# Optimization experiments

Hardware: AMD Instinct MI355X
Metric: run time of the kernel (lower is better)

Reference implementation:

```python
import jax, jax.numpy as jnp
import numpy as np

DEMBED = 512
DMODEL = 512
HEAD = 8
B, L = 4, 2048


def setup_inputs() -> dict:
    key = jax.random.key(0)
    ks = jax.random.split(key, 12)
    s_in = 1.0 / np.sqrt(DEMBED)
    s_out = 1.0 / np.sqrt(DMODEL)
    return {
        "x_q": jax.random.normal(ks[0], (B, L, DEMBED), jnp.float32),
        "x_k": jax.random.normal(ks[1], (B, L, DEMBED), jnp.float32),
        "x_v": jax.random.normal(ks[2], (B, L, DEMBED), jnp.float32),
        "mask": jax.random.randint(ks[3], (B, L, L), 0, 2, jnp.int32),
        "Wq": jax.random.uniform(ks[4], (DMODEL, DEMBED), jnp.float32, -s_in, s_in),
        "bq": jnp.zeros((DMODEL,), jnp.float32),
        "Wk": jax.random.uniform(ks[5], (DMODEL, DEMBED), jnp.float32, -s_in, s_in),
        "bk": jnp.zeros((DMODEL,), jnp.float32),
        "Wv": jax.random.uniform(ks[6], (DMODEL, DEMBED), jnp.float32, -s_in, s_in),
        "bv": jnp.zeros((DMODEL,), jnp.float32),
        "Wo": jax.random.uniform(ks[7], (DEMBED, DMODEL), jnp.float32, -s_out, s_out),
        "bo": jnp.zeros((DEMBED,), jnp.float32),
    }


def _split_heads(x):
    # [B, L, D] -> [B, head, L, h_dv]; head h gets contiguous channels h*h_dv:(h+1)*h_dv,
    # matching torch's transpose(1,2).reshape(B,head,h_dv,L).transpose(2,3)
    b, l, d = x.shape
    return x.reshape(b, l, HEAD, d // HEAD).transpose(0, 2, 1, 3)


def reference(x_q, x_k, x_v, mask, Wq, bq, Wk, bk, Wv, bv, Wo, bo):
    q = _split_heads(x_q @ Wq.T + bq)  # [B, H, L, hd]
    k = _split_heads(x_k @ Wk.T + bk)
    v = _split_heads(x_v @ Wv.T + bv)
    h_dv = q.shape[-1]
    scores = jnp.einsum("bhqd,bhkd->bhqk", q, k) / np.sqrt(h_dv)
    scores = scores + mask[:, None, :, :].astype(scores.dtype) * (-1e30)
    attn = jax.nn.softmax(scores, axis=-1)
    out = jnp.einsum("bhqk,bhkd->bhqd", attn, v)  # [B, H, L, hd]
    out = out.transpose(0, 2, 1, 3).reshape(x_q.shape[0], x_q.shape[1], DMODEL)
    final = out @ Wo.T + bo
    return final, attn
```

## Files before the change

### kernel.cpp

```cpp
#include <hip/hip_runtime.h>

typedef unsigned short u16;
typedef __attribute__((ext_vector_type(8))) short short8;
typedef __attribute__((ext_vector_type(4))) float f32x4;

#define DE 512
#define SL 2048
#define NB 4
#define NH 8
#define HD 64

__device__ __forceinline__ float bf2f(u16 h) {
    union { unsigned u; float f; } v; v.u = ((unsigned)h) << 16; return v.f;
}
__device__ __forceinline__ u16 f2bf(float f) {
    union { float f; unsigned u; } v; v.f = f;
    unsigned u = v.u;
    return (u16)((u + 0x7FFFu + ((u >> 16) & 1u)) >> 16);
}
__device__ __forceinline__ short8 ld8f(const float* __restrict__ p) {
    const float4 a = *(const float4*)p;
    const float4 b = *(const float4*)(p + 4);
    short8 r;
    ((u16*)&r)[0] = f2bf(a.x); ((u16*)&r)[1] = f2bf(a.y);
    ((u16*)&r)[2] = f2bf(a.z); ((u16*)&r)[3] = f2bf(a.w);
    ((u16*)&r)[4] = f2bf(b.x); ((u16*)&r)[5] = f2bf(b.y);
    ((u16*)&r)[6] = f2bf(b.z); ((u16*)&r)[7] = f2bf(b.w);
    return r;
}

__global__ __launch_bounds__(256) void cvt3(const float* __restrict__ s0,
                                            const float* __restrict__ s1,
                                            const float* __restrict__ s2,
                                            u16* __restrict__ dst, int per) {
    const float* src = (blockIdx.y == 0) ? s0 : ((blockIdx.y == 1) ? s1 : s2);
    const int idx = (blockIdx.x * 256 + threadIdx.x) * 8;
    if (idx >= per) return;
    short8 v = ld8f(src + idx);
    *(short8*)(dst + (size_t)blockIdx.y * per + idx) = v;
}

__device__ __forceinline__ void llds16(const u16* g, u16* l) {
    __builtin_amdgcn_global_load_lds((const __attribute__((address_space(1))) void*)g,
                                     (__attribute__((address_space(3))) void*)l, 16, 0, 0);
}

template <int MODE>
__global__ __launch_bounds__(256, 1) void gemm_lds(const u16* __restrict__ X,
                                                   const u16* __restrict__ W,
                                                   const float* __restrict__ bias,
                                                   void* __restrict__ outv) {
    __shared__ __align__(16) u16 As[2][8192];
    __shared__ __align__(16) u16 Bs[2][8192];

    const int tid = threadIdx.x;
    const int l = tid & 63, w = tid >> 6;
    const int q16 = l & 15, quad = l >> 4;
    const int tok0 = blockIdx.x * 128;
    const int col0 = blockIdx.y * 128;
    const int wr = w >> 1, wc = w & 1;

    const int srow = w * 8 + (l >> 3);
    const int scol = ((l & 7) ^ (l >> 3)) * 8;
    const u16* ga = X + (size_t)(tok0 + srow) * DE + scol;
    const u16* gb = W + (size_t)(col0 + srow) * DE + scol;
    u16* la0 = &As[0][tid * 8]; u16* la1 = &As[1][tid * 8];
    u16* lb0 = &Bs[0][tid * 8]; u16* lb1 = &Bs[1][tid * 8];

    f32x4 acc[4][4] = {};

    #pragma unroll
    for (int i = 0; i < 4; ++i) {
        llds16(ga + (size_t)i * 32 * DE, la0 + i * 2048);
        llds16(gb + (size_t)i * 32 * DE, lb0 + i * 2048);
    }
    __syncthreads();

    int cur = 0;
    for (int ks = 64; ks <= DE; ks += 64) {
        if (ks < DE) {
            u16* da = cur ? la0 : la1;
            u16* db = cur ? lb0 : lb1;
            #pragma unroll
            for (int i = 0; i < 4; ++i) {
                llds16(ga + (size_t)i * 32 * DE + ks, da + i * 2048);
                llds16(gb + (size_t)i * 32 * DE + ks, db + i * 2048);
            }
        }
        const char* Ab = (const char*)As[cur];
        const char* Bb = (const char*)Bs[cur];
        #pragma unroll
        for (int kk = 0; kk < 64; kk += 32) {
            short8 af[4], bf[4];
            #pragma unroll
            for (int m = 0; m < 4; ++m) {
                const int row = wr * 64 + m * 16 + q16;
                const int byt = row * 128 + (((kk + quad * 8) * 2) ^ ((q16 & 7) << 4));
                af[m] = *(const short8*)(Ab + byt);
            }
            #pragma unroll
            for (int n = 0; n < 4; ++n) {
                const int row = wc * 64 + n * 16 + q16;
                const int byt = row * 128 + (((kk + quad * 8) * 2) ^ ((q16 & 7) << 4));
                bf[n] = *(const short8*)(Bb + byt);
            }
            #pragma unroll
            for (int m = 0; m < 4; ++m)
                #pragma unroll
                for (int n = 0; n < 4; ++n)
                    acc[m][n] = __builtin_amdgcn_mfma_f32_16x16x32_bf16(af[m], bf[n], acc[m][n], 0, 0, 0);
        }
        __syncthreads();
        cur ^= 1;
    }

    #pragma unroll
    for (int n = 0; n < 4; ++n) {
        const int col = col0 + wc * 64 + n * 16 + q16;
        const float bv = bias[col];
        #pragma unroll
        for (int m = 0; m < 4; ++m) {
            const f32x4 a4 = acc[m][n];
            const int tg0 = tok0 + wr * 64 + m * 16 + quad * 4;
            if (MODE == 2) {
                const int b = tg0 >> 11, t0 = tg0 & 2047;
                const int h = col >> 6, d = col & 63;
                ushort4 pk;
                pk.x = f2bf(a4[0] + bv); pk.y = f2bf(a4[1] + bv);
                pk.z = f2bf(a4[2] + bv); pk.w = f2bf(a4[3] + bv);
                *(ushort4*)((u16*)outv + ((size_t)((b * NH + h) * HD + d) << 11) + t0) = pk;
            } else if (MODE == 1) {
                const int h = col >> 6, d = col & 63;
                #pragma unroll
                for (int r = 0; r < 4; ++r) {
                    const int tg = tg0 + r;
                    const int b = tg >> 11, t = tg & 2047;
                    ((u16*)outv)[(((size_t)(b * NH + h) * SL + t) << 6) + d] = f2bf(a4[r] + bv);
                }
            } else {
                #pragma unroll
                for (int r = 0; r < 4; ++r)
                    ((float*)outv)[(size_t)(tg0 + r) * DE + col] = a4[r] + bv;
            }
        }
    }
}

template <bool XBF, bool WBF, int MODE>
__global__ __launch_bounds__(256) void gemm512(const void* __restrict__ Xv,
                                               const void* __restrict__ Wv,
                                               const float* __restrict__ bias,
                                               void* __restrict__ outv) {
    const int lane = threadIdx.x & 63;
    const int wave = threadIdx.x >> 6;
    const int q16 = lane & 15, quad = lane >> 4;
    const int row0 = blockIdx.x * 64 + wave * 16;
    const int col0 = blockIdx.y * 64;

    f32x4 acc[4] = {};
    #pragma unroll 4
    for (int kk = 0; kk < DE; kk += 32) {
        short8 a;
        if (XBF)
            a = *(const short8*)((const u16*)Xv + (size_t)(row0 + q16) * DE + kk + quad * 8);
        else
            a = ld8f((const float*)Xv + (size_t)(row0 + q16) * DE + kk + quad * 8);
        #pragma unroll
        for (int ct = 0; ct < 4; ++ct) {
            short8 bw;
            if (WBF)
                bw = *(const short8*)((const u16*)Wv + (size_t)(col0 + ct * 16 + q16) * DE + kk + quad * 8);
            else
                bw = ld8f((const float*)Wv + (size_t)(col0 + ct * 16 + q16) * DE + kk + quad * 8);
            acc[ct] = __builtin_amdgcn_mfma_f32_16x16x32_bf16(a, bw, acc[ct], 0, 0, 0);
        }
    }
    #pragma unroll
    for (int ct = 0; ct < 4; ++ct) {
        const int col = col0 + ct * 16 + q16;
        const float bv = bias[col];
        #pragma unroll
        for (int r = 0; r < 4; ++r) {
            const int tg = row0 + quad * 4 + r;
            ((float*)outv)[(size_t)tg * DE + col] = acc[ct][r] + bv;
        }
    }
}

__global__ __launch_bounds__(512) void attn_kernel(const u16* __restrict__ Q,
                                                   const u16* __restrict__ K,
                                                   const u16* __restrict__ Vt,
                                                   const int* __restrict__ mask,
                                                   float* __restrict__ attn_out,
                                                   u16* __restrict__ Obuf) {
    __shared__ __align__(16) u16 P[16][2056];
    __shared__ float partial[16][8];
    __shared__ float linv[16];
    __shared__ float ored[4][16][16];

    const int tid = threadIdx.x;
    const int lane = tid & 63, wave = tid >> 6;
    const int q16 = lane & 15, quad = lane >> 4;
    const int qblk = blockIdx.x, h = blockIdx.y, b = blockIdx.z;
    const int qbase = qblk * 16;

    const u16* qplane = Q + (size_t)((b * NH + h) * SL) * HD;
    const u16* kplane = K + (size_t)((b * NH + h) * SL) * HD;

    const u16* qrow = qplane + (qbase + q16) * HD + quad * 8;
    const short8 aq0 = *(const short8*)(qrow);
    const short8 aq1 = *(const short8*)(qrow + 32);

    const int qg0 = qbase + quad * 4;
    const int* mbase = mask + (size_t)(b * SL + qg0) * SL;
    const int k0 = wave * 256;
    float rs0 = 0.f, rs1 = 0.f, rs2 = 0.f, rs3 = 0.f;
    #pragma unroll 2
    for (int kt = 0; kt < 16; ++kt) {
        const int kbase = k0 + kt * 16;
        const u16* krow = kplane + (kbase + q16) * HD + quad * 8;
        short8 b0 = *(const short8*)(krow);
        short8 b1 = *(const short8*)(krow + 32);
        f32x4 s = {};
        s = __builtin_amdgcn_mfma_f32_16x16x32_bf16(aq0, b0, s, 0, 0, 0);
        s = __builtin_amdgcn_mfma_f32_16x16x32_bf16(aq1, b1, s, 0, 0, 0);
        const int* mrow = mbase + kbase + q16;
        const float u0 = mrow[0]          ? 0.0f : __expf(s[0] * 0.125f);
        const float u1 = mrow[SL]         ? 0.0f : __expf(s[1] * 0.125f);
        const float u2 = mrow[2 * SL]     ? 0.0f : __expf(s[2] * 0.125f);
        const float u3 = mrow[3 * SL]     ? 0.0f : __expf(s[3] * 0.125f);
        rs0 += u0; rs1 += u1; rs2 += u2; rs3 += u3;
        P[quad * 4 + 0][kbase + q16] = f2bf(u0);
        P[quad * 4 + 1][kbase + q16] = f2bf(u1);
        P[quad * 4 + 2][kbase + q16] = f2bf(u2);
        P[quad * 4 + 3][kbase + q16] = f2bf(u3);
    }
    #pragma unroll
    for (int off = 1; off < 16; off <<= 1) {
        rs0 += __shfl_xor(rs0, off);
        rs1 += __shfl_xor(rs1, off);
        rs2 += __shfl_xor(rs2, off);
        rs3 += __shfl_xor(rs3, off);
    }
    if (q16 == 0) {
        partial[quad * 4 + 0][wave] = rs0;
        partial[quad * 4 + 1][wave] = rs1;
        partial[quad * 4 + 2][wave] = rs2;
        partial[quad * 4 + 3][wave] = rs3;
    }
    __syncthreads();

    if (tid < 16) {
        float s = 0.f;
        #pragma unroll
        for (int w = 0; w < 8; ++w) s += partial[tid][w];
        linv[tid] = 1.0f / s;
    }
    __syncthreads();

    {
        const int r3 = tid >> 5, cseg = tid & 31;
        const float inv = linv[r3];
        const size_t rowbase = ((size_t)((b * NH + h) * SL + qbase + r3)) * SL;
        #pragma unroll
        for (int i = 0; i < 8; ++i) {
            const int c = cseg * 8 + i * 256;
            short8 v = *(const short8*)&P[r3][c];
            f32x4 w0, w1;
            w0[0] = bf2f(((u16*)&v)[0]) * inv;
            w0[1] = bf2f(((u16*)&v)[1]) * inv;
            w0[2] = bf2f(((u16*)&v)[2]) * inv;
            w0[3] = bf2f(((u16*)&v)[3]) * inv;
            w1[0] = bf2f(((u16*)&v)[4]) * inv;
            w1[1] = bf2f(((u16*)&v)[5]) * inv;
            w1[2] = bf2f(((u16*)&v)[6]) * inv;
            w1[3] = bf2f(((u16*)&v)[7]) * inv;
            __builtin_nontemporal_store(w0, (f32x4*)(attn_out + rowbase + c));
            __builtin_nontemporal_store(w1, (f32x4*)(attn_out + rowbase + c + 4));
        }
    }

    const int dt = wave & 3, kh = wave >> 2;
    const u16* vplane = Vt + (size_t)((b * NH + h) * HD) * SL;
    f32x4 o = {};
    const int kstart = kh * 1024;
    #pragma unroll 4
    for (int kk = kstart; kk < kstart + 1024; kk += 32) {
        short8 a = *(const short8*)&P[q16][kk + quad * 8];
        short8 bv = *(const short8*)(vplane + (dt * 16 + q16) * SL + kk + quad * 8);
        o = __builtin_amdgcn_mfma_f32_16x16x32_bf16(a, bv, o, 0, 0, 0);
    }
    if (kh == 1) {
        #pragma unroll
        for (int rr = 0; rr < 4; ++rr) ored[dt][quad * 4 + rr][q16] = o[rr];
    }
    __syncthreads();
    if (kh == 0) {
        #pragma unroll
        for (int rr = 0; rr < 4; ++rr) {
            const int row = quad * 4 + rr;
            const float val = (o[rr] + ored[dt][row][q16]) * linv[row];
            const int qg = qbase + row;
            Obuf[(size_t)(b * SL + qg) * DE + h * HD + dt * 16 + q16] = f2bf(val);
        }
    }
}

extern "C" void kernel_launch(void* const* d_in, const int* in_sizes, int n_in,
                              void* d_out, int out_size, void* d_ws, size_t ws_size,
                              hipStream_t stream) {
    const float* x_q = (const float*)d_in[0];
    const float* x_k = (const float*)d_in[1];
    const float* x_v = (const float*)d_in[2];
    const int* mask = (const int*)d_in[3];
    const float* Wq = (const float*)d_in[4];
    const float* bq = (const float*)d_in[5];
    const float* Wk = (const float*)d_in[6];
    const float* bk = (const float*)d_in[7];
    const float* Wv = (const float*)d_in[8];
    const float* bv = (const float*)d_in[9];
    const float* Wo = (const float*)d_in[10];
    const float* bo = (const float*)d_in[11];

    u16* ws = (u16*)d_ws;
    u16* qb = ws;
    u16* kb = ws + 4194304;
    u16* vt = ws + 2 * 4194304;
    u16* ob = ws + 3 * 4194304;

    float* outp = (float*)d_out;
    float* attn_out = outp + 4194304;

    u16* xbf = (u16*)attn_out;
    u16* wbf = xbf + 3 * 4194304;

    cvt3<<<dim3(2048, 3), 256, 0, stream>>>(x_q, x_k, x_v, xbf, 4194304);
    cvt3<<<dim3(128, 3), 256, 0, stream>>>(Wq, Wk, Wv, wbf, 262144);

    dim3 gl(64, 4);
    gemm_lds<1><<<gl, 256, 0, stream>>>(xbf, wbf, bq, qb);
    gemm_lds<1><<<gl, 256, 0, stream>>>(xbf + 4194304, wbf + 262144, bk, kb);
    gemm_lds<2><<<gl, 256, 0, stream>>>(xbf + 2 * 4194304, wbf + 2 * 262144, bv, vt);

    attn_kernel<<<dim3(128, 8, 4), 512, 0, stream>>>(qb, kb, vt, mask, attn_out, ob);

    if (ws_size >= (size_t)34078720) {
        u16* wobf = ws + 4 * 4194304;
        cvt3<<<dim3(128, 1), 256, 0, stream>>>(Wo, Wo, Wo, wobf, 262144);
        gemm_lds<0><<<gl, 256, 0, stream>>>(ob, wobf, bo, outp);
    } else {
        gemm512<true, false, 0><<<dim3(128, 8), 256, 0, stream>>>(ob, Wo, bo, outp);
    }
}
```

Baseline: 891.0 us.

## Merge QKV projections into one launch with smaller 64x64 tiles

The three Q/K/V projection GEMMs become a single launch that uses blockIdx.z to pick the input, weight and bias. Output tiles shrink from 128x128 to 64x64, so each GEMM gets 1024 blocks instead of 256, and the launch-bounds minimum of one block per CU is dropped. The output projection now always uses the LDS-tiled bf16 path, with Wo converted into the freed Q buffer, replacing the older register-only fallback. The aim is to fill the GPU better and cut launch count, at the cost of lower per-block data reuse and more global traffic per FLOP.

```diff
diff --git a/kernel.cpp b/kernel.cpp
--- a/kernel.cpp
+++ b/kernel.cpp
@@ -45,69 +45,63 @@
                                      (__attribute__((address_space(3))) void*)l, 16, 0, 0);
 }
 
-template <int MODE>
-__global__ __launch_bounds__(256, 1) void gemm_lds(const u16* __restrict__ X,
-                                                   const u16* __restrict__ W,
-                                                   const float* __restrict__ bias,
-                                                   void* __restrict__ outv) {
-    __shared__ __align__(16) u16 As[2][8192];
-    __shared__ __align__(16) u16 Bs[2][8192];
-
+__device__ __forceinline__ void gemm64_body(u16* As, u16* Bs,
+                                            const u16* __restrict__ X,
+                                            const u16* __restrict__ W,
+                                            const float* __restrict__ bias,
+                                            void* __restrict__ outv,
+                                            int mode, int tok0, int col0) {
     const int tid = threadIdx.x;
     const int l = tid & 63, w = tid >> 6;
     const int q16 = l & 15, quad = l >> 4;
-    const int tok0 = blockIdx.x * 128;
-    const int col0 = blockIdx.y * 128;
     const int wr = w >> 1, wc = w & 1;
 
-    const int srow = w * 8 + (l >> 3);
-    const int scol = ((l & 7) ^ (l >> 3)) * 8;
+    const int srow = tid >> 3;
+    const int scol = ((tid & 7) ^ (srow & 7)) * 8;
     const u16* ga = X + (size_t)(tok0 + srow) * DE + scol;
     const u16* gb = W + (size_t)(col0 + srow) * DE + scol;
-    u16* la0 = &As[0][tid * 8]; u16* la1 = &As[1][tid * 8];
-    u16* lb0 = &Bs[0][tid * 8]; u16* lb1 = &Bs[1][tid * 8];
-
-    f32x4 acc[4][4] = {};
+    u16* la = As + tid * 8;
+    u16* lb = Bs + tid * 8;
+
+    f32x4 acc[2][2] = {};
 
     #pragma unroll
-    for (int i = 0; i < 4; ++i) {
-        llds16(ga + (size_t)i * 32 * DE, la0 + i * 2048);
-        llds16(gb + (size_t)i * 32 * DE, lb0 + i * 2048);
+    for (int i = 0; i < 2; ++i) {
+        llds16(ga + (size_t)i * 32 * DE, la + i * 2048);
+        llds16(gb + (size_t)i * 32 * DE, lb + i * 2048);
     }
     __syncthreads();
 
     int cur = 0;
     for (int ks = 64; ks <= DE; ks += 64) {
         if (ks < DE) {
-            u16* da = cur ? la0 : la1;
-            u16* db = cur ? lb0 : lb1;
+            u16* da = la + (cur ^ 1) * 4096;
+            u16* db = lb + (cur ^ 1) * 4096;
             #pragma unroll
-            for (int i = 0; i < 4; ++i) {
+            for (int i = 0; i < 2; ++i) {
                 llds16(ga + (size_t)i * 32 * DE + ks, da + i * 2048);
                 llds16(gb + (size_t)i * 32 * DE + ks, db + i * 2048);
             }
         }
-        const char* Ab = (const char*)As[cur];
-        const char* Bb = (const char*)Bs[cur];
+        const char* Ab = (const char*)(As + cur * 4096);
+        const char* Bb = (const char*)(Bs + cur * 4096);
         #pragma unroll
         for (int kk = 0; kk < 64; kk += 32) {
-            short8 af[4], bf[4];
+            short8 af[2], bf[2];
             #pragma unroll
-            for (int m = 0; m < 4; ++m) {
-                const int row = wr * 64 + m * 16 + q16;
-                const int byt = row * 128 + (((kk + quad * 8) * 2) ^ ((q16 & 7) << 4));
-                af[m] = *(const short8*)(Ab + byt);
+            for (int m = 0; m < 2; ++m) {
+                const int row = wr * 32 + m * 16 + q16;
+                af[m] = *(const short8*)(Ab + row * 128 + (((kk + quad * 8) * 2) ^ ((q16 & 7) << 4)));
             }
             #pragma unroll
-            for (int n = 0; n < 4; ++n) {
-                const int row = wc * 64 + n * 16 + q16;
-                const int byt = row * 128 + (((kk + quad * 8) * 2) ^ ((q16 & 7) << 4));
-                bf[n] = *(const short8*)(Bb + byt);
+            for (int n = 0; n < 2; ++n) {
+                const int row = wc * 32 + n * 16 + q16;
+                bf[n] = *(const short8*)(Bb + row * 128 + (((kk + quad * 8) * 2) ^ ((q16 & 7) << 4)));
             }
             #pragma unroll
-            for (int m = 0; m < 4; ++m)
+            for (int m = 0; m < 2; ++m)
                 #pragma unroll
-                for (int n = 0; n < 4; ++n)
+                for (int n = 0; n < 2; ++n)
                     acc[m][n] = __builtin_amdgcn_mfma_f32_16x16x32_bf16(af[m], bf[n], acc[m][n], 0, 0, 0);
         }
         __syncthreads();
@@ -115,21 +109,21 @@
     }
 
     #pragma unroll
-    for (int n = 0; n < 4; ++n) {
-        const int col = col0 + wc * 64 + n * 16 + q16;
+    for (int n = 0; n < 2; ++n) {
+        const int col = col0 + wc * 32 + n * 16 + q16;
         const float bv = bias[col];
         #pragma unroll
-        for (int m = 0; m < 4; ++m) {
+        for (int m = 0; m < 2; ++m) {
             const f32x4 a4 = acc[m][n];
-            const int tg0 = tok0 + wr * 64 + m * 16 + quad * 4;
-            if (MODE == 2) {
+            const int tg0 = tok0 + wr * 32 + m * 16 + quad * 4;
+            if (mode == 2) {
                 const int b = tg0 >> 11, t0 = tg0 & 2047;
                 const int h = col >> 6, d = col & 63;
                 ushort4 pk;
                 pk.x = f2bf(a4[0] + bv); pk.y = f2bf(a4[1] + bv);
                 pk.z = f2bf(a4[2] + bv); pk.w = f2bf(a4[3] + bv);
                 *(ushort4*)((u16*)outv + ((size_t)((b * NH + h) * HD + d) << 11) + t0) = pk;
-            } else if (MODE == 1) {
+            } else if (mode == 1) {
                 const int h = col >> 6, d = col & 63;
                 #pragma unroll
                 for (int r = 0; r < 4; ++r) {
@@ -146,45 +140,31 @@
     }
 }
 
-template <bool XBF, bool WBF, int MODE>
-__global__ __launch_bounds__(256) void gemm512(const void* __restrict__ Xv,
-                                               const void* __restrict__ Wv,
-                                               const float* __restrict__ bias,
-                                               void* __restrict__ outv) {
-    const int lane = threadIdx.x & 63;
-    const int wave = threadIdx.x >> 6;
-    const int q16 = lane & 15, quad = lane >> 4;
-    const int row0 = blockIdx.x * 64 + wave * 16;
-    const int col0 = blockIdx.y * 64;
-
-    f32x4 acc[4] = {};
-    #pragma unroll 4
-    for (int kk = 0; kk < DE; kk += 32) {
-        short8 a;
-        if (XBF)
-            a = *(const short8*)((const u16*)Xv + (size_t)(row0 + q16) * DE + kk + quad * 8);
-        else
-            a = ld8f((const float*)Xv + (size_t)(row0 + q16) * DE + kk + quad * 8);
-        #pragma unroll
-        for (int ct = 0; ct < 4; ++ct) {
-            short8 bw;
-            if (WBF)
-                bw = *(const short8*)((const u16*)Wv + (size_t)(col0 + ct * 16 + q16) * DE + kk + quad * 8);
-            else
-                bw = ld8f((const float*)Wv + (size_t)(col0 + ct * 16 + q16) * DE + kk + quad * 8);
-            acc[ct] = __builtin_amdgcn_mfma_f32_16x16x32_bf16(a, bw, acc[ct], 0, 0, 0);
-        }
-    }
-    #pragma unroll
-    for (int ct = 0; ct < 4; ++ct) {
-        const int col = col0 + ct * 16 + q16;
-        const float bv = bias[col];
-        #pragma unroll
-        for (int r = 0; r < 4; ++r) {
-            const int tg = row0 + quad * 4 + r;
-            ((float*)outv)[(size_t)tg * DE + col] = acc[ct][r] + bv;
-        }
-    }
+__global__ __launch_bounds__(256) void gemm_qkv(const u16* __restrict__ xbf,
+                                                const u16* __restrict__ wbf,
+                                                const float* __restrict__ bq,
+                                                const float* __restrict__ bk,
+                                                const float* __restrict__ bv,
+                                                u16* __restrict__ outbase) {
+    __shared__ __align__(16) u16 As[2][4096];
+    __shared__ __align__(16) u16 Bs[2][4096];
+    const int z = blockIdx.z;
+    const u16* X = xbf + (size_t)z * 4194304;
+    const u16* W = wbf + (size_t)z * 262144;
+    const float* bias = (z == 0) ? bq : ((z == 1) ? bk : bv);
+    u16* out = outbase + (size_t)z * 4194304;
+    gemm64_body(&As[0][0], &Bs[0][0], X, W, bias, out,
+                (z == 2) ? 2 : 1, blockIdx.x * 64, blockIdx.y * 64);
+}
+
+__global__ __launch_bounds__(256) void gemm_fin(const u16* __restrict__ X,
+                                                const u16* __restrict__ W,
+                                                const float* __restrict__ bias,
+                                                float* __restrict__ outp) {
+    __shared__ __align__(16) u16 As[2][4096];
+    __shared__ __align__(16) u16 Bs[2][4096];
+    gemm64_body(&As[0][0], &Bs[0][0], X, W, bias, outp,
+                0, blockIdx.x * 64, blockIdx.y * 64);
 }
 
 __global__ __launch_bounds__(512) void attn_kernel(const u16* __restrict__ Q,
@@ -324,7 +304,6 @@
 
     u16* ws = (u16*)d_ws;
     u16* qb = ws;
-    u16* kb = ws + 4194304;
     u16* vt = ws + 2 * 4194304;
     u16* ob = ws + 3 * 4194304;
 
@@ -337,18 +316,10 @@
     cvt3<<<dim3(2048, 3), 256, 0, stream>>>(x_q, x_k, x_v, xbf, 4194304);
     cvt3<<<dim3(128, 3), 256, 0, stream>>>(Wq, Wk, Wv, wbf, 262144);
 
-    dim3 gl(64, 4);
-    gemm_lds<1><<<gl, 256, 0, stream>>>(xbf, wbf, bq, qb);
-    gemm_lds<1><<<gl, 256, 0, stream>>>(xbf + 4194304, wbf + 262144, bk, kb);
-    gemm_lds<2><<<gl, 256, 0, stream>>>(xbf + 2 * 4194304, wbf + 2 * 262144, bv, vt);
-
-    attn_kernel<<<dim3(128, 8, 4), 512, 0, stream>>>(qb, kb, vt, mask, attn_out, ob);
-
-    if (ws_size >= (size_t)34078720) {
-        u16* wobf = ws + 4 * 4194304;
-        cvt3<<<dim3(128, 1), 256, 0, stream>>>(Wo, Wo, Wo, wobf, 262144);
-        gemm_lds<0><<<gl, 256, 0, stream>>>(ob, wobf, bo, outp);
-    } else {
-        gemm512<true, false, 0><<<dim3(128, 8), 256, 0, stream>>>(ob, Wo, bo, outp);
-    }
-}
+    gemm_qkv<<<dim3(128, 8, 3), 256, 0, stream>>>(xbf, wbf, bq, bk, bv, ws);
+
+    attn_kernel<<<dim3(128, 8, 4), 512, 0, stream>>>(qb, ws + 4194304, vt, mask, attn_out, ob);
+
+    cvt3<<<dim3(128, 1), 256, 0, stream>>>(Wo, Wo, Wo, qb, 262144);
+    gemm_fin<<<dim3(128, 8), 256, 0, stream>>>(ob, qb, bo, outp);
+}
```

After: 880.1 us. Within noise of the previous version (-1.2%).
